# Optimization experiments

Measured on AMD Instinct MI355X. Metric: run time of the kernel, lower is better.

## Reference

```python
import jax, jax.numpy as jnp
import numpy as np

PATCH = 96
VOL = 192
STRIDE = 48
C = 2
B = 1
GD = 48  # global low-res grid


def _gaussian_wt(p):
    # MONAI-style gaussian importance map: delta at center (p//2), sigma = 0.125*p,
    # separable gaussian product, normalized so max == 1.
    i = jnp.arange(p, dtype=jnp.float32)
    c = jnp.float32(p // 2)
    sigma = jnp.float32(0.125 * p)
    g = jnp.exp(-0.5 * ((i - c) / sigma) ** 2)
    w = g[:, None, None] * g[None, :, None] * g[None, None, :]  # [p,p,p]
    return w / w.max()


def setup_inputs() -> dict:
    key = jax.random.key(0)
    k1, k2 = jax.random.split(key)
    # deterministic overlapping patch grid (stride 48, patch 96, vol 192 -> 3 per axis)
    pos = list(range(0, VOL - PATCH + 1, STRIDE))
    starts = np.array([[d, h, w] for d in pos for h in pos for w in pos], dtype=np.int32)  # [27,3]
    K = starts.shape[0]
    patch_logits = jax.random.normal(k1, (K * B, C, PATCH, PATCH, PATCH), dtype=jnp.float32)
    global_logit = jax.random.normal(k2, (B, C, GD, GD, GD), dtype=jnp.float32)
    return {
        "patch_logits": patch_logits,
        "global_logit": global_logit,
        "patch_starts": jnp.asarray(starts),
    }


def reference(patch_logits, global_logit, patch_starts):
    K, Cc, P = patch_logits.shape[0], patch_logits.shape[1], patch_logits.shape[2]
    V = VOL
    wt = _gaussian_wt(P)  # [P,P,P], matches fixed_wt buffer

    offs = jnp.arange(P, dtype=jnp.int32)
    dd = patch_starts[:, 0][:, None] + offs  # [K,P]
    hh = patch_starts[:, 1][:, None] + offs
    ww = patch_starts[:, 2][:, None] + offs
    # flattened voxel index per patch element: [K,P,P,P]
    flat = ((dd[:, :, None, None] * V + hh[:, None, :, None]) * V + ww[:, None, None, :]).reshape(-1)

    # weighted scatter-add of all patches (batch=1 so all patches target batch 0)
    vals = (patch_logits * wt[None, None]).transpose(1, 0, 2, 3, 4).reshape(Cc, -1)  # [C, K*P^3]
    final = jnp.zeros((Cc, V * V * V), patch_logits.dtype).at[:, flat].add(vals)

    wvals = jnp.broadcast_to(wt, (K, P, P, P)).reshape(-1)
    wmap = jnp.full((V * V * V,), 1e-20, patch_logits.dtype).at[flat].add(wvals)
    mask = jnp.zeros((V * V * V,), patch_logits.dtype).at[flat].set(1.0)

    # trilinear upsample, align_corners=False (half-pixel) == jax.image.resize linear
    up = jax.image.resize(global_logit, (B, Cc, V, V, V), method='trilinear')

    out = (final / wmap).reshape(B, Cc, V, V, V)
    out = out + jnp.where(mask.reshape(B, 1, V, V, V) == 1.0, 0.0, up)
    return out
```

## Files before the change

kernel.cpp:

```cpp
#include <hip/hip_runtime.h>


constexpr int V   = 192;
constexpr int P   = 96;
constexpr int S   = 48;
constexpr int NC  = 2;
constexpr int QPR = V / 4;
constexpr int NQ  = NC * V * V * QPR;

__global__ __launch_bounds__(256) void
DynamicPatchAggregator_85418309583422_kernel(const float* __restrict__ patches,
                                             float* __restrict__ out)
{
    __shared__ __align__(16) float sg[P];
    if (threadIdx.x < P) {
        float t = ((float)(int)threadIdx.x - 48.0f) * (1.0f / 12.0f);
        sg[threadIdx.x] = __expf(-0.5f * t * t);
    }
    __syncthreads();
    const float4* sg4 = reinterpret_cast<const float4*>(sg);

    int idx = blockIdx.x * 256 + threadIdx.x;

    int wq = idx % QPR;
    int t1 = idx / QPR;
    int h  = t1 % V;
    int t2 = t1 / V;
    int d  = t2 % V;
    int c  = t2 / V;
    int w  = wq * 4;

    int kd_lo = max(0, (d - S) / S), kd_hi = min(2, d / S);
    int kh_lo = max(0, (h - S) / S), kh_hi = min(2, h / S);
    int kw_lo = max(0, (w - S) / S), kw_hi = min(2, w / S);

    float Gd = 0.0f, Gh = 0.0f;
    for (int kd = kd_lo; kd <= kd_hi; ++kd) Gd += sg[d - kd * S];
    for (int kh = kh_lo; kh <= kh_hi; ++kh) Gh += sg[h - kh * S];

    float4 acc = make_float4(0.0f, 0.0f, 0.0f, 0.0f);
    float4 Gw  = make_float4(0.0f, 0.0f, 0.0f, 0.0f);

    for (int kw = kw_lo; kw <= kw_hi; ++kw) {
        int pwq = wq - kw * (S / 4);
        float4 g4 = sg4[pwq];
        Gw.x += g4.x; Gw.y += g4.y; Gw.z += g4.z; Gw.w += g4.w;
        int pw = pwq * 4;
        for (int kd = kd_lo; kd <= kd_hi; ++kd) {
            int   pd  = d - kd * S;
            float gdk = sg[pd];
            for (int kh = kh_lo; kh <= kh_hi; ++kh) {
                int ph = h - kh * S;
                float a = gdk * sg[ph];
                int k   = (kd * 3 + kh) * 3 + kw;
                int off = (((k * NC + c) * P + pd) * P + ph) * P + pw;
                float4 pv = *reinterpret_cast<const float4*>(patches + off);
                acc.x += (a * g4.x) * pv.x;
                acc.y += (a * g4.y) * pv.y;
                acc.z += (a * g4.z) * pv.z;
                acc.w += (a * g4.w) * pv.w;
            }
        }
    }

    float GdGh = Gd * Gh;
    float4 o;
    o.x = acc.x / (GdGh * Gw.x + 1e-20f);
    o.y = acc.y / (GdGh * Gw.y + 1e-20f);
    o.z = acc.z / (GdGh * Gw.z + 1e-20f);
    o.w = acc.w / (GdGh * Gw.w + 1e-20f);

    reinterpret_cast<float4*>(out)[idx] = o;
}

extern "C" void kernel_launch(void* const* d_in, const int* in_sizes, int n_in,
                              void* d_out, int out_size, void* d_ws, size_t ws_size,
                              hipStream_t stream) {
    const float* patches = (const float*)d_in[0];
    float* out = (float*)d_out;

    DynamicPatchAggregator_85418309583422_kernel<<<NQ / 256, 256, 0, stream>>>(patches, out);
}
```

Baseline: 284.7 us.

## Stage contributing patch rows in shared memory per (c,d,8-row) block tile

New measurement: 309.6 us. +8.8%, slower.

```diff
diff --git a/kernel.cpp b/kernel.cpp
--- a/kernel.cpp
+++ b/kernel.cpp
@@ -1,76 +1,125 @@
 #include <hip/hip_runtime.h>
 
 
-constexpr int V   = 192;
-constexpr int P   = 96;
-constexpr int S   = 48;
-constexpr int NC  = 2;
-constexpr int QPR = V / 4;
-constexpr int NQ  = NC * V * V * QPR;
+constexpr int V  = 192;
+constexpr int P  = 96;
+constexpr int S  = 48;
+constexpr int NC = 2;
+constexpr int TH = 8;
+constexpr int NT = 384;
+constexpr int CF4 = TH * P / 4;
+constexpr int NBLK = NC * V * (V / TH);
 
-__global__ __launch_bounds__(256) void
+__global__ __launch_bounds__(NT) void
 DynamicPatchAggregator_85418309583422_kernel(const float* __restrict__ patches,
                                              float* __restrict__ out)
 {
-    __shared__ __align__(16) float sg[P];
-    if (threadIdx.x < P) {
-        float t = ((float)(int)threadIdx.x - 48.0f) * (1.0f / 12.0f);
-        sg[threadIdx.x] = __expf(-0.5f * t * t);
+    __shared__ __align__(16) float  sg[P];
+    __shared__ __align__(16) float4 stage[12 * CF4];
+
+    const int t = threadIdx.x;
+    if (t < P) {
+        float x = ((float)(t - 48)) * (1.0f / 12.0f);
+        sg[t] = __expf(-0.5f * x * x);
+    }
+
+    const int bid = blockIdx.x;
+    const int ht  = bid % (V / TH);
+    const int d   = (bid / (V / TH)) % V;
+    const int c   = bid / ((V / TH) * V);
+    const int H0  = ht * TH;
+
+    const int dq  = d / S;
+    const int kd0 = max(0, dq - 1);
+    const int nkd = (dq == 1 || dq == 2) ? 2 : 1;
+    const int hq  = H0 / S;
+    const int kh0 = max(0, hq - 1);
+    const int nkh = (hq == 1 || hq == 2) ? 2 : 1;
+
+    const int nchunk = nkd * nkh * 3;
+    const int total  = nchunk * CF4;
+    for (int base = t; base < total; base += 4 * NT) {
+        float4 v[4];
+        int   su[4];
+        int nv = 0;
+#pragma unroll
+        for (int q = 0; q < 4; ++q) {
+            const int u = base + q * NT;
+            if (u < total) {
+                const int chunk = u / CF4;
+                const int r     = u % CF4;
+                const int kw = chunk % 3;
+                const int j  = (chunk / 3) % nkh;
+                const int i  = chunk / (3 * nkh);
+                const int kd = kd0 + i, kh = kh0 + j;
+                const int pd  = d  - kd * S;
+                const int ph0 = H0 - kh * S;
+                const int k   = (kd * 3 + kh) * 3 + kw;
+                const int off = (((k * NC + c) * P + pd) * P + ph0) * P;
+                v[q]  = reinterpret_cast<const float4*>(patches + off)[r];
+                su[q] = ((i * 2 + j) * 3 + kw) * CF4 + r;
+                nv = q + 1;
+            }
+        }
+#pragma unroll
+        for (int q = 0; q < 4; ++q)
+            if (q < nv) stage[su[q]] = v[q];
     }
     __syncthreads();
-    const float4* sg4 = reinterpret_cast<const float4*>(sg);
 
-    int idx = blockIdx.x * 256 + threadIdx.x;
+    const int hl = t / 48;
+    const int w4 = t % 48;
+    const int h  = H0 + hl;
 
-    int wq = idx % QPR;
-    int t1 = idx / QPR;
-    int h  = t1 % V;
-    int t2 = t1 / V;
-    int d  = t2 % V;
-    int c  = t2 / V;
-    int w  = wq * 4;
+    const int  wr  = w4 / 12;
+    const int  kwa = max(0, wr - 1);
+    const bool wv  = (wr == 1) | (wr == 2);
+    const int  kwb = wv ? kwa + 1 : kwa;
+    const int  pqa = w4 - kwa * 12;
+    const int  pqb = wv ? pqa - 12 : pqa;
+    const float4 gwa = reinterpret_cast<const float4*>(sg)[pqa];
+    float4 gwb = reinterpret_cast<const float4*>(sg)[pqb];
+    if (!wv) gwb = make_float4(0.0f, 0.0f, 0.0f, 0.0f);
 
-    int kd_lo = max(0, (d - S) / S), kd_hi = min(2, d / S);
-    int kh_lo = max(0, (h - S) / S), kh_hi = min(2, h / S);
-    int kw_lo = max(0, (w - S) / S), kw_hi = min(2, w / S);
+    const float gd0 = sg[d - kd0 * S];
+    const float gd1 = (nkd == 2) ? sg[d - (kd0 + 1) * S] : 0.0f;
+    const float gh0 = sg[h - kh0 * S];
+    const float gh1 = (nkh == 2) ? sg[h - (kh0 + 1) * S] : 0.0f;
 
-    float Gd = 0.0f, Gh = 0.0f;
-    for (int kd = kd_lo; kd <= kd_hi; ++kd) Gd += sg[d - kd * S];
-    for (int kh = kh_lo; kh <= kh_hi; ++kh) Gh += sg[h - kh * S];
+    const float gdA[2] = {gd0, gd1};
+    const float ghA[2] = {gh0, gh1};
+    const int   iA[2]  = {0, nkd - 1};
+    const int   jA[2]  = {0, nkh - 1};
+    const int   kwA[2] = {kwa, kwb};
+    const int   pqA[2] = {pqa, pqb};
+    const float4 gwA[2] = {gwa, gwb};
 
     float4 acc = make_float4(0.0f, 0.0f, 0.0f, 0.0f);
-    float4 Gw  = make_float4(0.0f, 0.0f, 0.0f, 0.0f);
-
-    for (int kw = kw_lo; kw <= kw_hi; ++kw) {
-        int pwq = wq - kw * (S / 4);
-        float4 g4 = sg4[pwq];
-        Gw.x += g4.x; Gw.y += g4.y; Gw.z += g4.z; Gw.w += g4.w;
-        int pw = pwq * 4;
-        for (int kd = kd_lo; kd <= kd_hi; ++kd) {
-            int   pd  = d - kd * S;
-            float gdk = sg[pd];
-            for (int kh = kh_lo; kh <= kh_hi; ++kh) {
-                int ph = h - kh * S;
-                float a = gdk * sg[ph];
-                int k   = (kd * 3 + kh) * 3 + kw;
-                int off = (((k * NC + c) * P + pd) * P + ph) * P + pw;
-                float4 pv = *reinterpret_cast<const float4*>(patches + off);
-                acc.x += (a * g4.x) * pv.x;
-                acc.y += (a * g4.y) * pv.y;
-                acc.z += (a * g4.z) * pv.z;
-                acc.w += (a * g4.w) * pv.w;
+#pragma unroll
+    for (int i = 0; i < 2; ++i)
+#pragma unroll
+        for (int j = 0; j < 2; ++j) {
+            const float a = gdA[i] * ghA[j];
+#pragma unroll
+            for (int k = 0; k < 2; ++k) {
+                const float4 pv =
+                    stage[((iA[i] * 2 + jA[j]) * 3 + kwA[k]) * CF4 + hl * 24 + pqA[k]];
+                const float4 g = gwA[k];
+                acc.x += (a * g.x) * pv.x;
+                acc.y += (a * g.y) * pv.y;
+                acc.z += (a * g.z) * pv.z;
+                acc.w += (a * g.w) * pv.w;
             }
         }
-    }
 
-    float GdGh = Gd * Gh;
+    const float GdGh = (gd0 + gd1) * (gh0 + gh1);
     float4 o;
-    o.x = acc.x / (GdGh * Gw.x + 1e-20f);
-    o.y = acc.y / (GdGh * Gw.y + 1e-20f);
-    o.z = acc.z / (GdGh * Gw.z + 1e-20f);
-    o.w = acc.w / (GdGh * Gw.w + 1e-20f);
+    o.x = acc.x / (GdGh * (gwa.x + gwb.x) + 1e-20f);
+    o.y = acc.y / (GdGh * (gwa.y + gwb.y) + 1e-20f);
+    o.z = acc.z / (GdGh * (gwa.z + gwb.z) + 1e-20f);
+    o.w = acc.w / (GdGh * (gwa.w + gwb.w) + 1e-20f);
 
-    reinterpret_cast<float4*>(out)[idx] = o;
+    reinterpret_cast<float4*>(out)[bid * NT + t] = o;
 }
 
 extern "C" void kernel_launch(void* const* d_in, const int* in_sizes, int n_in,
@@ -79,5 +128,5 @@
     const float* patches = (const float*)d_in[0];
     float* out = (float*)d_out;
 
-    DynamicPatchAggregator_85418309583422_kernel<<<NQ / 256, 256, 0, stream>>>(patches, out);
+    DynamicPatchAggregator_85418309583422_kernel<<<NBLK, NT, 0, stream>>>(patches, out);
 }
```
